# Kernel optimization log

Measured on AMD Instinct MI355X. Metric: run time of the kernel, lower is better.

Reference implementation:

```python
import jax, jax.numpy as jnp
import numpy as np

N_NODES = 20000
N_EDGES = 320000
N_GRAPHS = 256
D = 256
L = 4
EPS = 1e-5


def setup_inputs() -> dict:
    key = jax.random.key(0)
    ks = jax.random.split(key, 20)
    x = jax.random.normal(ks[0], (N_NODES, D), dtype=jnp.float32)
    edge_index = jax.random.randint(ks[1], (2, N_EDGES), 0, N_NODES, dtype=jnp.int64)
    batch = jnp.sort(jax.random.randint(ks[2], (N_NODES,), 0, N_GRAPHS, dtype=jnp.int64))
    s = 1.0 / np.sqrt(D)
    Wl = jax.random.uniform(ks[3], (L, D, D), jnp.float32, -s, s)
    bl = jax.random.uniform(ks[4], (L, D), jnp.float32, -s, s)
    Wr = jax.random.uniform(ks[5], (L, D, D), jnp.float32, -s, s)
    gamma = jnp.ones((L, D), jnp.float32)
    beta = jnp.zeros((L, D), jnp.float32)
    fc1_w = jax.random.uniform(ks[6], (D, 128), jnp.float32, -s, s)
    fc1_b = jax.random.uniform(ks[7], (128,), jnp.float32, -s, s)
    s2 = 1.0 / np.sqrt(128)
    fc2_w = jax.random.uniform(ks[8], (128, 64), jnp.float32, -s2, s2)
    fc2_b = jax.random.uniform(ks[9], (64,), jnp.float32, -s2, s2)
    s3 = 1.0 / np.sqrt(64)
    fc3_w = jax.random.uniform(ks[10], (64, 10), jnp.float32, -s3, s3)
    fc3_b = jax.random.uniform(ks[11], (10,), jnp.float32, -s3, s3)
    return dict(x=x, edge_index=edge_index, batch=batch, Wl=Wl, bl=bl, Wr=Wr,
                gamma=gamma, beta=beta, fc1_w=fc1_w, fc1_b=fc1_b,
                fc2_w=fc2_w, fc2_b=fc2_b, fc3_w=fc3_w, fc3_b=fc3_b)


def reference(x, edge_index, batch, Wl, bl, Wr, gamma, beta,
              fc1_w, fc1_b, fc2_w, fc2_b, fc3_w, fc3_b):
    src, dst = edge_index[0], edge_index[1]
    # in-degree for mean aggregation (zero-degree nodes -> 0 aggregate)
    deg = jax.ops.segment_sum(jnp.ones((src.shape[0],), x.dtype), dst, num_segments=N_NODES)
    inv_deg = jnp.where(deg > 0, 1.0 / jnp.maximum(deg, 1.0), 0.0)[:, None]
    for i in range(L):
        # SAGEConv: mean-aggregate neighbors, then lin_l(agg) + lin_r(x)
        agg = jax.ops.segment_sum(x[src], dst, num_segments=N_NODES) * inv_deg
        h = agg @ Wl[i] + bl[i] + x @ Wr[i]
        # BatchNorm (training mode: biased batch statistics over nodes)
        mu = jnp.mean(h, axis=0)
        var = jnp.mean(jnp.square(h - mu), axis=0)
        h = (h - mu) * jax.lax.rsqrt(var + EPS) * gamma[i] + beta[i]
        x = jax.nn.relu(h)
    # global_mean_pool over graphs
    cnt = jax.ops.segment_sum(jnp.ones((N_NODES,), x.dtype), batch, num_segments=N_GRAPHS)
    g = jax.ops.segment_sum(x, batch, num_segments=N_GRAPHS) / jnp.maximum(cnt, 1.0)[:, None]
    # MLP classifier: 256 -> 128 -> 64 -> 10
    g = jax.nn.relu(g @ fc1_w + fc1_b)
    g = jax.nn.relu(g @ fc2_w + fc2_b)
    return g @ fc3_w + fc3_b
```

## Files before the change

kernel.cpp:

```cpp
#include <hip/hip_runtime.h>
#include <hip/hip_bf16.h>

#define NN 20000
#define NE 320000
#define NG 256
#define DD 256
#define NL 4
#define NBX2 157
#define NBKT 79

typedef __attribute__((ext_vector_type(8))) short short8;
typedef __attribute__((ext_vector_type(4))) float float4_t;

__device__ __forceinline__ int ld_idx(const int* __restrict__ p, int i, int f64) {
    return f64 ? p[2 * i] : p[i];
}

__device__ __forceinline__ float bf2f(ushort u) {
    return __uint_as_float(((unsigned)u) << 16);
}

__device__ __forceinline__ ushort f2bf(float f) {
    __hip_bfloat16 b = __float2bfloat16(f);
    return *(ushort*)&b;
}


__global__ void k_init(const int* __restrict__ ei, const int* __restrict__ batch,
                       const ushort* __restrict__ x, int* __restrict__ flags,
                       int* __restrict__ deg) {
    int gid = blockIdx.x * 256 + threadIdx.x;
    for (int i = gid; i < NN; i += gridDim.x * 256) deg[i] = 0;
    if (blockIdx.x == 0) {
        __shared__ int cnt0, cnt1, weird;
        int t = threadIdx.x;
        if (t == 0) { cnt0 = 0; cnt1 = 0; weird = 0; }
        __syncthreads();
        for (int tt = t; tt < 512; tt += 256) {
            if (ei[2 * tt + 1] != 0) atomicAdd(&cnt0, 1);
            int i = tt * 9;
            if (batch[2 * i + 1] != 0) atomicAdd(&cnt1, 1);
#pragma unroll
            for (int j = 0; j < 16; j++) {
                ushort v = x[tt * 16 + j];
                if (((v >> 7) & 0xFF) >= 0xC0) atomicAdd(&weird, 1);
            }
        }
        __syncthreads();
        if (t == 0) {
            flags[0] = (cnt0 == 0) ? 1 : 0;
            flags[1] = (cnt1 == 0) ? 1 : 0;
            flags[2] = (weird == 0) ? 1 : 0;
        }
    }
}


#define POFF_BL   0
#define POFF_GA   1024
#define POFF_BE   2048
#define POFF_F1W  3072
#define POFF_F1B  35840
#define POFF_F2W  35968
#define POFF_F2B  44160
#define POFF_F3W  44224
#define POFF_F3B  44864
#define PTOT      44874

#define NB_CVT8   2500
#define NB_FRAG   2048
#define NB_CVTP   176
#define NB_DEG    1250
#define NB_GST    79
#define B_FRAG    (NB_CVT8)
#define B_CVTP    (B_FRAG + NB_FRAG)
#define B_DEG     (B_CVTP + NB_CVTP)
#define B_GST     (B_DEG + NB_DEG)
#define NB_PREP   (B_GST + NB_GST)


__global__ __launch_bounds__(256) void k_prep(
    const void* __restrict__ x_in, const void* __restrict__ WL,
    const void* __restrict__ WR, const int* __restrict__ ei,
    const int* __restrict__ batch,
    const void* s0, const void* s1, const void* s2, const void* s3,
    const void* s4, const void* s5, const void* s6, const void* s7, const void* s8,
    ushort* __restrict__ xcan, ushort* __restrict__ wtL, ushort* __restrict__ wtR,
    ushort* __restrict__ pcan, int* __restrict__ deg, int* __restrict__ gstart,
    const int* __restrict__ fl) {
    int blk = blockIdx.x;
    int t = threadIdx.x;
    if (blk < B_FRAG) {
        int i = blk * 256 + t;
        if (fl[2]) {
            *(int4*)(xcan + (size_t)i * 8) = ((const int4*)x_in)[i];
        } else {
            const float* f = (const float*)x_in + (size_t)i * 8;
            ushort ov[8];
#pragma unroll
            for (int d = 0; d < 8; d++) ov[d] = f2bf(f[d]);
            *(int4*)(xcan + (size_t)i * 8) = *(int4*)ov;
        }
    } else if (blk < B_CVTP) {
        int idx = (blk - B_FRAG) * 256 + t;
        int half = idx >> 18;
        int id = idx & 0x3FFFF;
        int within = id & 0xFFFF;
        int lmat = id >> 16;
        int fblk = within >> 9;
        int lane = (within >> 3) & 63;
        int e = within & 7;
        int n = (fblk >> 3) * 16 + (lane & 15);
        int k = (fblk & 7) * 32 + (lane >> 4) * 8 + e;
        const void* W = half ? WR : WL;
        ushort* Wt = half ? wtR : wtL;
        size_t src = ((size_t)lmat << 16) + (k << 8) + n;
        Wt[id] = fl[2] ? ((const ushort*)W)[src] : f2bf(((const float*)W)[src]);
    } else if (blk < B_DEG) {
        int i = (blk - B_CVTP) * 256 + t;
        if (i >= PTOT) return;
        const int offs[10] = {POFF_BL, POFF_GA, POFF_BE, POFF_F1W, POFF_F1B,
                              POFF_F2W, POFF_F2B, POFF_F3W, POFF_F3B, PTOT};
        const void* srcs[9] = {s0, s1, s2, s3, s4, s5, s6, s7, s8};
        int seg = 0;
#pragma unroll
        for (int k = 1; k < 9; k++) if (i >= offs[k]) seg = k;
        int local = i - offs[seg];
        if (fl[2]) pcan[i] = ((const ushort*)srcs[seg])[local];
        else       pcan[i] = f2bf(((const float*)srcs[seg])[local]);
    } else if (blk < B_GST) {
        int e = (blk - B_DEG) * 256 + t;
        if (e < NE) {
            int src = ld_idx(ei, e, fl[0]);
            int dst = ld_idx(ei, NE + e, fl[0]);
            if ((unsigned)dst < NN && (unsigned)src < NN) atomicAdd(&deg[dst], 1);
        }
    } else {
        int i = (blk - B_GST) * 256 + t;
        if (i >= NN) return;
        int b = ld_idx(batch, i, fl[1]);
        int bp = (i == 0) ? -1 : ld_idx(batch, i - 1, fl[1]);
        for (int g = bp + 1; g <= b; g++)
            if ((unsigned)g <= NG) gstart[g] = i;
        if (i == NN - 1)
            for (int g = b + 1; g <= NG; g++) gstart[g] = NN;
    }
}


__global__ __launch_bounds__(256) void k_scanA(const int* __restrict__ deg,
                                               int* __restrict__ bsum) {
    __shared__ int red[256];
    int t = threadIdx.x;
    int node = blockIdx.x * 256 + t;
    red[t] = (node < NN) ? deg[node] : 0;
    __syncthreads();
    for (int off = 128; off; off >>= 1) {
        if (t < off) red[t] += red[t + off];
        __syncthreads();
    }
    if (t == 0) bsum[blockIdx.x] = red[0];
}

__global__ __launch_bounds__(128) void k_scanB(const int* __restrict__ bsum,
                                               int* __restrict__ bpref,
                                               int* __restrict__ rowst) {
    __shared__ int part[128];
    int t = threadIdx.x;
    int s = (t < NBKT) ? bsum[t] : 0;
    part[t] = s;
    __syncthreads();
    for (int off = 1; off < 128; off <<= 1) {
        int v = (t >= off) ? part[t - off] : 0;
        __syncthreads();
        part[t] += v;
        __syncthreads();
    }
    if (t < NBKT) bpref[t] = part[t] - s;
    if (t == NBKT - 1) { bpref[NBKT] = part[t]; rowst[NN] = part[t]; }
}

__global__ __launch_bounds__(256) void k_scanC(
    const int* __restrict__ deg, const int* __restrict__ bpref,
    int* __restrict__ rowst, int* __restrict__ cursor, float* __restrict__ invdeg) {
    __shared__ int part[256];
    int b = blockIdx.x, t = threadIdx.x;
    int node = b * 256 + t;
    int d = (node < NN) ? deg[node] : 0;
    part[t] = d;
    __syncthreads();
    for (int off = 1; off < 256; off <<= 1) {
        int v = (t >= off) ? part[t - off] : 0;
        __syncthreads();
        part[t] += v;
        __syncthreads();
    }
    if (node < NN) {
        int o = bpref[b] + part[t] - d;
        rowst[node] = o;
        cursor[node] = o;
        invdeg[node] = d > 0 ? 1.0f / (float)d : 0.0f;
    }
}

__global__ void k_fill(const int* __restrict__ ei, int* __restrict__ cursor,
                       int* __restrict__ csr, const int* __restrict__ fl) {
    int e = blockIdx.x * 256 + threadIdx.x;
    if (e < NE) {
        int src = ld_idx(ei, e, fl[0]);
        int dst = ld_idx(ei, NE + e, fl[0]);
        if ((unsigned)dst < NN && (unsigned)src < NN) {
            int p = atomicAdd(&cursor[dst], 1);
            if ((unsigned)p < NE) csr[p] = src;
        }
    }
}


template <int BNF>
__global__ __launch_bounds__(256) void k_agg4(
    const ushort* __restrict__ X, const int* __restrict__ rs,
    const int* __restrict__ csr, const float* __restrict__ invdeg,
    const float* __restrict__ bnsc, const float* __restrict__ bnsh,
    ushort* __restrict__ AGG) {
    int node = blockIdx.x * 4 + (threadIdx.x >> 6);
    if (node >= NN) return;
    int h = (threadIdx.x >> 5) & 1;
    int j = threadIdx.x & 31;
    float sc[8], sh[8];
    if (BNF) {
        float4 a0 = *(const float4*)(bnsc + j * 8);
        float4 a1 = *(const float4*)(bnsc + j * 8 + 4);
        float4 b0 = *(const float4*)(bnsh + j * 8);
        float4 b1 = *(const float4*)(bnsh + j * 8 + 4);
        sc[0] = a0.x; sc[1] = a0.y; sc[2] = a0.z; sc[3] = a0.w;
        sc[4] = a1.x; sc[5] = a1.y; sc[6] = a1.z; sc[7] = a1.w;
        sh[0] = b0.x; sh[1] = b0.y; sh[2] = b0.z; sh[3] = b0.w;
        sh[4] = b1.x; sh[5] = b1.y; sh[6] = b1.z; sh[7] = b1.w;
    }
    int e0 = rs[node], e1 = rs[node + 1];
    float acc[8] = {};
    int e = e0 + h;
    for (; e + 14 < e1; e += 16) {
        int4 v[8];
#pragma unroll
        for (int r = 0; r < 8; r++) {
            int s = csr[e + 2 * r];
            v[r] = *(const int4*)(X + (size_t)s * DD + j * 8);
        }
#pragma unroll
        for (int r = 0; r < 8; r++) {
            const ushort* u = (const ushort*)&v[r];
#pragma unroll
            for (int d = 0; d < 8; d++) {
                float x = bf2f(u[d]);
                if (BNF) x = fmaxf(x * sc[d] + sh[d], 0.0f);
                acc[d] += x;
            }
        }
    }
    for (; e + 2 < e1; e += 4) {
        int sA = csr[e], sB = csr[e + 2];
        int4 vA = *(const int4*)(X + (size_t)sA * DD + j * 8);
        int4 vB = *(const int4*)(X + (size_t)sB * DD + j * 8);
        const ushort* uA = (const ushort*)&vA;
        const ushort* uB = (const ushort*)&vB;
#pragma unroll
        for (int d = 0; d < 8; d++) {
            float xA = bf2f(uA[d]), xB = bf2f(uB[d]);
            if (BNF) {
                xA = fmaxf(xA * sc[d] + sh[d], 0.0f);
                xB = fmaxf(xB * sc[d] + sh[d], 0.0f);
            }
            acc[d] += xA + xB;
        }
    }
    for (; e < e1; e += 2) {
        int s = csr[e];
        int4 v = *(const int4*)(X + (size_t)s * DD + j * 8);
        const ushort* u = (const ushort*)&v;
#pragma unroll
        for (int d = 0; d < 8; d++) {
            float x = bf2f(u[d]);
            if (BNF) x = fmaxf(x * sc[d] + sh[d], 0.0f);
            acc[d] += x;
        }
    }
#pragma unroll
    for (int d = 0; d < 8; d++)
        acc[d] += __shfl_down(acc[d], 32);
    if (h == 0) {
        float inv = invdeg[node];
        ushort ov[8];
#pragma unroll
        for (int d = 0; d < 8; d++) ov[d] = f2bf(acc[d] * inv);
        *(int4*)(AGG + (size_t)node * DD + j * 8) = *(int4*)ov;
    }
}


template <int BNF>
__global__ __launch_bounds__(256) void k_gemm5(
    const ushort* __restrict__ A1, const ushort* __restrict__ A2,
    const ushort* __restrict__ WtF1, const ushort* __restrict__ WtF2,
    const ushort* __restrict__ bias,
    const float* __restrict__ bnsc, const float* __restrict__ bnsh,
    ushort* __restrict__ H, float* __restrict__ psum, float* __restrict__ psq) {
    __shared__ ushort Als[128][40];
    __shared__ float colsum[128];
    __shared__ float colsq[128];
    const int m0 = blockIdx.x * 128;
    const int n0 = blockIdx.y * 128;
    const int tid = threadIdx.x;
    const int w = tid >> 6, l = tid & 63, lr = l & 15, q = l >> 4;
    const int wm = (w >> 1) * 64, wn = (w & 1) * 64;
    float4_t acc[4][4] = {};

    const int srow = tid >> 1;
    const int sce = (tid & 1) * 16;
    const int nb8 = ((n0 + wn) >> 4) * 8;

    for (int mat = 0; mat < 2; ++mat) {
        const ushort* A = mat ? A2 : A1;
        const ushort* Wf = mat ? WtF2 : WtF1;
        for (int k0 = 0; k0 < 256; k0 += 32) {
            int ar = m0 + srow; if (ar >= NN) ar = NN - 1;
            int4 av0 = *(const int4*)(A + (size_t)ar * DD + k0 + sce);
            int4 av1 = *(const int4*)(A + (size_t)ar * DD + k0 + sce + 8);
            if (BNF && mat == 1) {
                float scv[16], shv[16];
#pragma unroll
                for (int g = 0; g < 4; g++) {
                    float4 s4 = *(const float4*)(bnsc + k0 + sce + g * 4);
                    float4 h4 = *(const float4*)(bnsh + k0 + sce + g * 4);
                    scv[g*4] = s4.x; scv[g*4+1] = s4.y; scv[g*4+2] = s4.z; scv[g*4+3] = s4.w;
                    shv[g*4] = h4.x; shv[g*4+1] = h4.y; shv[g*4+2] = h4.z; shv[g*4+3] = h4.w;
                }
                ushort* u0 = (ushort*)&av0;
                ushort* u1 = (ushort*)&av1;
#pragma unroll
                for (int d = 0; d < 8; d++) {
                    u0[d] = f2bf(fmaxf(bf2f(u0[d]) * scv[d] + shv[d], 0.0f));
                    u1[d] = f2bf(fmaxf(bf2f(u1[d]) * scv[8 + d] + shv[8 + d], 0.0f));
                }
            }
            *(int4*)&Als[srow][sce] = av0;
            *(int4*)&Als[srow][sce + 8] = av1;
            const ushort* bbase = Wf + (((size_t)(nb8 + (k0 >> 5))) << 9) + l * 8;
            short8 bf[4];
#pragma unroll
            for (int in = 0; in < 4; in++)
                bf[in] = *(const short8*)(bbase + in * 4096);
            __syncthreads();
            short8 af[4];
#pragma unroll
            for (int im = 0; im < 4; im++)
                af[im] = *(const short8*)&Als[wm + im * 16 + lr][q * 8];
#pragma unroll
            for (int im = 0; im < 4; im++)
#pragma unroll
                for (int in = 0; in < 4; in++)
                    acc[im][in] = __builtin_amdgcn_mfma_f32_16x16x32_bf16(
                        af[im], bf[in], acc[im][in], 0, 0, 0);
            __syncthreads();
        }
    }
    if (tid < 128) { colsum[tid] = 0.0f; colsq[tid] = 0.0f; }
    __syncthreads();

    int mbase = m0 + wm + q * 4;
#pragma unroll
    for (int in = 0; in < 4; in++) {
        int n = n0 + wn + in * 16 + lr;
        float b = bf2f(bias[n]);
        float s = 0.0f, s2 = 0.0f;
#pragma unroll
        for (int im = 0; im < 4; im++) {
#pragma unroll
            for (int i = 0; i < 4; i++) {
                int m = mbase + im * 16 + i;
                if (m < NN) {
                    float hv = acc[im][in][i] + b;
                    ushort hb = f2bf(hv);
                    H[(size_t)m * DD + n] = hb;
                    float hq = bf2f(hb);
                    s += hq;
                    s2 += hq * hq;
                }
            }
        }
        s += __shfl_xor(s, 16);  s += __shfl_xor(s, 32);
        s2 += __shfl_xor(s2, 16); s2 += __shfl_xor(s2, 32);
        if (q == 0) {
            atomicAdd(&colsum[wn + in * 16 + lr], s);
            atomicAdd(&colsq[wn + in * 16 + lr], s2);
        }
    }
    __syncthreads();
    if (tid < 128) {
        psum[(size_t)blockIdx.x * DD + n0 + tid] = colsum[tid];
        psq[(size_t)blockIdx.x * DD + n0 + tid] = colsq[tid];
    }
}


__global__ __launch_bounds__(64) void k_bnfinal3(
    const float* __restrict__ psum, const float* __restrict__ psq,
    const ushort* __restrict__ gamma, const ushort* __restrict__ beta,
    float* __restrict__ scale, float* __restrict__ shift) {
    int c = blockIdx.x;
    int t = threadIdx.x;
    float s = 0.0f, s2 = 0.0f;
    for (int b = t; b < NBX2; b += 64) {
        s += psum[(size_t)b * DD + c];
        s2 += psq[(size_t)b * DD + c];
    }
#pragma unroll
    for (int o = 32; o; o >>= 1) {
        s += __shfl_down(s, o);
        s2 += __shfl_down(s2, o);
    }
    if (t == 0) {
        float mu = s * (1.0f / NN);
        float var = s2 * (1.0f / NN) - mu * mu;
        if (var < 0.0f) var = 0.0f;
        float rstd = rsqrtf(var + 1e-5f);
        float g = bf2f(gamma[c]);
        float b2 = bf2f(beta[c]);
        scale[c] = g * rstd;
        shift[c] = b2 - mu * g * rstd;
    }
}


__global__ __launch_bounds__(256) void k_head(
    const ushort* __restrict__ Hb, const float* __restrict__ scale,
    const float* __restrict__ shift, const int* __restrict__ gstart,
    const ushort* __restrict__ fc1w, const ushort* __restrict__ fc1b,
    const ushort* __restrict__ fc2w, const ushort* __restrict__ fc2b,
    const ushort* __restrict__ fc3w, const ushort* __restrict__ fc3b,
    void* __restrict__ out, const int* __restrict__ fl) {
    __shared__ float g[256];
    __shared__ float h1[128];
    __shared__ float h2[64];
    int gid = blockIdx.x;
    int t = threadIdx.x;
    int s0 = gstart[gid], e = gstart[gid + 1];
    float sc = scale[t], sh = shift[t];
    float acc = 0.0f;
    for (int i = s0; i < e; i++)
        acc += fmaxf(bf2f(Hb[(size_t)i * DD + t]) * sc + sh, 0.0f);
    g[t] = acc / fmaxf((float)(e - s0), 1.0f);
    __syncthreads();
    if (t < 128) {
        float a = bf2f(fc1b[t]);
        for (int k = 0; k < 256; k++)
            a += g[k] * bf2f(fc1w[k * 128 + t]);
        h1[t] = fmaxf(a, 0.0f);
    }
    __syncthreads();
    if (t < 64) {
        float a2 = bf2f(fc2b[t]);
        for (int k = 0; k < 128; k++)
            a2 += h1[k] * bf2f(fc2w[k * 64 + t]);
        h2[t] = fmaxf(a2, 0.0f);
    }
    __syncthreads();
    if (t < 10) {
        float a3 = bf2f(fc3b[t]);
        for (int k = 0; k < 64; k++)
            a3 += h2[k] * bf2f(fc3w[k * 10 + t]);
        if (fl[2]) ((__hip_bfloat16*)out)[gid * 10 + t] = __float2bfloat16(a3);
        else       ((float*)out)[gid * 10 + t] = a3;
    }
}


static inline char* bump(char*& p, size_t n) {
    char* r = p;
    p += (n + 255) & ~(size_t)255;
    return r;
}

extern "C" void kernel_launch(void* const* d_in, const int* in_sizes, int n_in,
                              void* d_out, int out_size, void* d_ws, size_t ws_size,
                              hipStream_t stream) {
    const void* x_in  = d_in[0];
    const int*  ei    = (const int*)d_in[1];
    const int*  batch = (const int*)d_in[2];
    const void* Wl    = d_in[3];
    const void* bl    = d_in[4];
    const void* Wr    = d_in[5];
    const void* gamma = d_in[6];
    const void* beta  = d_in[7];

    char* p = (char*)d_ws;
    int*    flags    = (int*)bump(p, 256);
    ushort* wtL      = (ushort*)bump(p, (size_t)NL * 65536 * 2);
    ushort* wtR      = (ushort*)bump(p, (size_t)NL * 65536 * 2);
    ushort* xcan     = (ushort*)bump(p, (size_t)NN * DD * 2);
    ushort* pcan     = (ushort*)bump(p, (size_t)PTOT * 2);
    int*    deg      = (int*)bump(p, NN * 4);
    int*    bsum     = (int*)bump(p, NBKT * 4);
    int*    bpref    = (int*)bump(p, (NBKT + 1) * 4);
    int*    rowst    = (int*)bump(p, (NN + 1) * 4);
    int*    cursor   = (int*)bump(p, NN * 4);
    float*  invdeg   = (float*)bump(p, NN * 4);
    int*    csr      = (int*)bump(p, NE * 4);
    int*    gstart   = (int*)bump(p, (NG + 1) * 4);
    ushort* agg      = (ushort*)bump(p, (size_t)NN * DD * 2);
    ushort* hb0      = (ushort*)bump(p, (size_t)NN * DD * 2);
    ushort* hb1      = (ushort*)bump(p, (size_t)NN * DD * 2);
    float*  psum     = (float*)bump(p, (size_t)NBX2 * DD * 4);
    float*  psq      = (float*)bump(p, (size_t)NBX2 * DD * 4);
    float*  scale    = (float*)bump(p, DD * 4);
    float*  shift    = (float*)bump(p, DD * 4);

    if ((size_t)(p - (char*)d_ws) > ws_size) return;

    ushort* blc = pcan + POFF_BL;
    ushort* gac = pcan + POFF_GA;
    ushort* bec = pcan + POFF_BE;
    ushort* f1w = pcan + POFF_F1W;
    ushort* f1b = pcan + POFF_F1B;
    ushort* f2w = pcan + POFF_F2W;
    ushort* f2b = pcan + POFF_F2B;
    ushort* f3w = pcan + POFF_F3W;
    ushort* f3b = pcan + POFF_F3B;

    k_init<<<80, 256, 0, stream>>>(ei, batch, (const ushort*)x_in, flags, deg);
    k_prep<<<NB_PREP, 256, 0, stream>>>(
        x_in, Wl, Wr, ei, batch,
        bl, gamma, beta, d_in[8], d_in[9], d_in[10], d_in[11], d_in[12], d_in[13],
        xcan, wtL, wtR, pcan, deg, gstart, flags);
    k_scanA<<<NBKT, 256, 0, stream>>>(deg, bsum);
    k_scanB<<<1, 128, 0, stream>>>(bsum, bpref, rowst);
    k_scanC<<<NBKT, 256, 0, stream>>>(deg, bpref, rowst, cursor, invdeg);
    k_fill<<<(NE + 255) / 256, 256, 0, stream>>>(ei, cursor, csr, flags);

    ushort* hbuf[2] = {hb0, hb1};
    const ushort* xsrc = xcan;
    for (int l = 0; l < NL; l++) {
        ushort* hdst = hbuf[l & 1];
        if (l == 0) {
            k_agg4<0><<<(NN + 3) / 4, 256, 0, stream>>>(xsrc, rowst, csr, invdeg,
                                                        scale, shift, agg);
            k_gemm5<0><<<dim3(NBX2, 2), 256, 0, stream>>>(
                agg, xsrc, wtL, wtR, blc, scale, shift, hdst, psum, psq);
        } else {
            k_agg4<1><<<(NN + 3) / 4, 256, 0, stream>>>(xsrc, rowst, csr, invdeg,
                                                        scale, shift, agg);
            k_gemm5<1><<<dim3(NBX2, 2), 256, 0, stream>>>(
                agg, xsrc, wtL + (size_t)l * 65536, wtR + (size_t)l * 65536,
                blc + l * DD, scale, shift, hdst, psum, psq);
        }
        k_bnfinal3<<<DD, 64, 0, stream>>>(psum, psq, gac + l * DD, bec + l * DD,
                                          scale, shift);
        xsrc = hdst;
    }

    k_head<<<NG, 256, 0, stream>>>(xsrc, scale, shift, gstart,
                                   f1w, f1b, f2w, f2b, f3w, f3b, d_out, flags);
}
```

Measured before the change: 372.5 us.

## Split aggregation across feature-column blocks and fold block-sum scan into scanC

The aggregation kernel now covers a 64-column slice per block, with a grid dimension of 4 slices. Within each wavefront, 8 groups of 8 lanes each take different edges and are reduced with xor shuffles, replacing two halves of 32 lanes over the full row. This puts more edges in flight per node and launches more blocks, at the cost of reading CSR indices four times and a longer shuffle reduction. The single-block scanB kernel is removed by having every scanC block redundantly scan the 79 block sums, which saves one launch.

```diff
diff --git a/kernel.cpp b/kernel.cpp
--- a/kernel.cpp
+++ b/kernel.cpp
@@ -162,29 +162,26 @@
     if (t == 0) bsum[blockIdx.x] = red[0];
 }
 
-__global__ __launch_bounds__(128) void k_scanB(const int* __restrict__ bsum,
-                                               int* __restrict__ bpref,
-                                               int* __restrict__ rowst) {
-    __shared__ int part[128];
-    int t = threadIdx.x;
-    int s = (t < NBKT) ? bsum[t] : 0;
-    part[t] = s;
-    __syncthreads();
-    for (int off = 1; off < 128; off <<= 1) {
-        int v = (t >= off) ? part[t - off] : 0;
-        __syncthreads();
-        part[t] += v;
-        __syncthreads();
-    }
-    if (t < NBKT) bpref[t] = part[t] - s;
-    if (t == NBKT - 1) { bpref[NBKT] = part[t]; rowst[NN] = part[t]; }
-}
-
 __global__ __launch_bounds__(256) void k_scanC(
-    const int* __restrict__ deg, const int* __restrict__ bpref,
+    const int* __restrict__ deg, const int* __restrict__ bsum,
     int* __restrict__ rowst, int* __restrict__ cursor, float* __restrict__ invdeg) {
+    __shared__ int bpart[128];
     __shared__ int part[256];
     int b = blockIdx.x, t = threadIdx.x;
+    if (t < 128) {
+        int s = (t < NBKT) ? bsum[t] : 0;
+        bpart[t] = s;
+    }
+    __syncthreads();
+    for (int off = 1; off < 128; off <<= 1) {
+        int v = 0;
+        if (t < 128 && t >= off) v = bpart[t - off];
+        __syncthreads();
+        if (t < 128) bpart[t] += v;
+        __syncthreads();
+    }
+    int bpref = (b == 0) ? 0 : bpart[b - 1];
+    if (b == 0 && t == 0) rowst[NN] = bpart[NBKT - 1];
     int node = b * 256 + t;
     int d = (node < NN) ? deg[node] : 0;
     part[t] = d;
@@ -196,7 +193,7 @@
         __syncthreads();
     }
     if (node < NN) {
-        int o = bpref[b] + part[t] - d;
+        int o = bpref + part[t] - d;
         rowst[node] = o;
         cursor[node] = o;
         invdeg[node] = d > 0 ? 1.0f / (float)d : 0.0f;
@@ -218,21 +215,23 @@
 
 
 template <int BNF>
-__global__ __launch_bounds__(256) void k_agg4(
+__global__ __launch_bounds__(256) void k_agg5(
     const ushort* __restrict__ X, const int* __restrict__ rs,
     const int* __restrict__ csr, const float* __restrict__ invdeg,
     const float* __restrict__ bnsc, const float* __restrict__ bnsh,
     ushort* __restrict__ AGG) {
     int node = blockIdx.x * 4 + (threadIdx.x >> 6);
     if (node >= NN) return;
-    int h = (threadIdx.x >> 5) & 1;
-    int j = threadIdx.x & 31;
+    int lane = threadIdx.x & 63;
+    int g = lane >> 3;
+    int j = lane & 7;
+    int cb = blockIdx.y * 64 + j * 8;
     float sc[8], sh[8];
     if (BNF) {
-        float4 a0 = *(const float4*)(bnsc + j * 8);
-        float4 a1 = *(const float4*)(bnsc + j * 8 + 4);
-        float4 b0 = *(const float4*)(bnsh + j * 8);
-        float4 b1 = *(const float4*)(bnsh + j * 8 + 4);
+        float4 a0 = *(const float4*)(bnsc + cb);
+        float4 a1 = *(const float4*)(bnsc + cb + 4);
+        float4 b0 = *(const float4*)(bnsh + cb);
+        float4 b1 = *(const float4*)(bnsh + cb + 4);
         sc[0] = a0.x; sc[1] = a0.y; sc[2] = a0.z; sc[3] = a0.w;
         sc[4] = a1.x; sc[5] = a1.y; sc[6] = a1.z; sc[7] = a1.w;
         sh[0] = b0.x; sh[1] = b0.y; sh[2] = b0.z; sh[3] = b0.w;
@@ -240,29 +239,11 @@
     }
     int e0 = rs[node], e1 = rs[node + 1];
     float acc[8] = {};
-    int e = e0 + h;
-    for (; e + 14 < e1; e += 16) {
-        int4 v[8];
-#pragma unroll
-        for (int r = 0; r < 8; r++) {
-            int s = csr[e + 2 * r];
-            v[r] = *(const int4*)(X + (size_t)s * DD + j * 8);
-        }
-#pragma unroll
-        for (int r = 0; r < 8; r++) {
-            const ushort* u = (const ushort*)&v[r];
-#pragma unroll
-            for (int d = 0; d < 8; d++) {
-                float x = bf2f(u[d]);
-                if (BNF) x = fmaxf(x * sc[d] + sh[d], 0.0f);
-                acc[d] += x;
-            }
-        }
-    }
-    for (; e + 2 < e1; e += 4) {
-        int sA = csr[e], sB = csr[e + 2];
-        int4 vA = *(const int4*)(X + (size_t)sA * DD + j * 8);
-        int4 vB = *(const int4*)(X + (size_t)sB * DD + j * 8);
+    int e = e0 + g;
+    for (; e + 8 < e1; e += 16) {
+        int sA = csr[e], sB = csr[e + 8];
+        int4 vA = *(const int4*)(X + (size_t)sA * DD + cb);
+        int4 vB = *(const int4*)(X + (size_t)sB * DD + cb);
         const ushort* uA = (const ushort*)&vA;
         const ushort* uB = (const ushort*)&vB;
 #pragma unroll
@@ -275,9 +256,9 @@
             acc[d] += xA + xB;
         }
     }
-    for (; e < e1; e += 2) {
+    for (; e < e1; e += 8) {
         int s = csr[e];
-        int4 v = *(const int4*)(X + (size_t)s * DD + j * 8);
+        int4 v = *(const int4*)(X + (size_t)s * DD + cb);
         const ushort* u = (const ushort*)&v;
 #pragma unroll
         for (int d = 0; d < 8; d++) {
@@ -287,14 +268,17 @@
         }
     }
 #pragma unroll
-    for (int d = 0; d < 8; d++)
-        acc[d] += __shfl_down(acc[d], 32);
-    if (h == 0) {
+    for (int d = 0; d < 8; d++) {
+        acc[d] += __shfl_xor(acc[d], 8);
+        acc[d] += __shfl_xor(acc[d], 16);
+        acc[d] += __shfl_xor(acc[d], 32);
+    }
+    if (g == 0) {
         float inv = invdeg[node];
         ushort ov[8];
 #pragma unroll
         for (int d = 0; d < 8; d++) ov[d] = f2bf(acc[d] * inv);
-        *(int4*)(AGG + (size_t)node * DD + j * 8) = *(int4*)ov;
+        *(int4*)(AGG + (size_t)node * DD + cb) = *(int4*)ov;
     }
 }
 
@@ -502,7 +486,6 @@
     ushort* pcan     = (ushort*)bump(p, (size_t)PTOT * 2);
     int*    deg      = (int*)bump(p, NN * 4);
     int*    bsum     = (int*)bump(p, NBKT * 4);
-    int*    bpref    = (int*)bump(p, (NBKT + 1) * 4);
     int*    rowst    = (int*)bump(p, (NN + 1) * 4);
     int*    cursor   = (int*)bump(p, NN * 4);
     float*  invdeg   = (float*)bump(p, NN * 4);
@@ -534,8 +517,7 @@
         bl, gamma, beta, d_in[8], d_in[9], d_in[10], d_in[11], d_in[12], d_in[13],
         xcan, wtL, wtR, pcan, deg, gstart, flags);
     k_scanA<<<NBKT, 256, 0, stream>>>(deg, bsum);
-    k_scanB<<<1, 128, 0, stream>>>(bsum, bpref, rowst);
-    k_scanC<<<NBKT, 256, 0, stream>>>(deg, bpref, rowst, cursor, invdeg);
+    k_scanC<<<NBKT, 256, 0, stream>>>(deg, bsum, rowst, cursor, invdeg);
     k_fill<<<(NE + 255) / 256, 256, 0, stream>>>(ei, cursor, csr, flags);
 
     ushort* hbuf[2] = {hb0, hb1};
@@ -543,13 +525,13 @@
     for (int l = 0; l < NL; l++) {
         ushort* hdst = hbuf[l & 1];
         if (l == 0) {
-            k_agg4<0><<<(NN + 3) / 4, 256, 0, stream>>>(xsrc, rowst, csr, invdeg,
-                                                        scale, shift, agg);
+            k_agg5<0><<<dim3((NN + 3) / 4, 4), 256, 0, stream>>>(
+                xsrc, rowst, csr, invdeg, scale, shift, agg);
             k_gemm5<0><<<dim3(NBX2, 2), 256, 0, stream>>>(
                 agg, xsrc, wtL, wtR, blc, scale, shift, hdst, psum, psq);
         } else {
-            k_agg4<1><<<(NN + 3) / 4, 256, 0, stream>>>(xsrc, rowst, csr, invdeg,
-                                                        scale, shift, agg);
+            k_agg5<1><<<dim3((NN + 3) / 4, 4), 256, 0, stream>>>(
+                xsrc, rowst, csr, invdeg, scale, shift, agg);
             k_gemm5<1><<<dim3(NBX2, 2), 256, 0, stream>>>(
                 agg, xsrc, wtL + (size_t)l * 65536, wtR + (size_t)l * 65536,
                 blc + l * DD, scale, shift, hdst, psum, psq);
```

After: 398.1 us. +6.9%, slower.

## Transpose weights via shared-memory tiles and fold block-sum scan into scanC

Applied to the files above, without the earlier changes.

The weight re-layout into MFMA fragment order changes from one scattered element per thread to 64x64 tiles staged through LDS. Each tile is read with coalesced loads and written back as 16-byte vectors, which cuts the prep blocks from 2048 to 128. The single-block scanB kernel is removed, and every scanC block now redundantly scans the 79 block sums in shared memory, saving one kernel launch and its serialization. The trade-off is extra LDS use and __syncthreads in k_prep and a small amount of duplicated scan work per block.

```diff
diff --git a/kernel.cpp b/kernel.cpp
--- a/kernel.cpp
+++ b/kernel.cpp
@@ -68,7 +68,7 @@
 #define PTOT      44874
 
 #define NB_CVT8   2500
-#define NB_FRAG   2048
+#define NB_FRAG   128
 #define NB_CVTP   176
 #define NB_DEG    1250
 #define NB_GST    79
@@ -102,20 +102,37 @@
             *(int4*)(xcan + (size_t)i * 8) = *(int4*)ov;
         }
     } else if (blk < B_CVTP) {
-        int idx = (blk - B_FRAG) * 256 + t;
-        int half = idx >> 18;
-        int id = idx & 0x3FFFF;
-        int within = id & 0xFFFF;
-        int lmat = id >> 16;
-        int fblk = within >> 9;
-        int lane = (within >> 3) & 63;
-        int e = within & 7;
-        int n = (fblk >> 3) * 16 + (lane & 15);
-        int k = (fblk & 7) * 32 + (lane >> 4) * 8 + e;
-        const void* W = half ? WR : WL;
-        ushort* Wt = half ? wtR : wtL;
-        size_t src = ((size_t)lmat << 16) + (k << 8) + n;
-        Wt[id] = fl[2] ? ((const ushort*)W)[src] : f2bf(((const float*)W)[src]);
+        __shared__ ushort T[64][65];
+        int bid = blk - B_FRAG;
+        int lm = bid >> 4;
+        int tile = bid & 15;
+        int tk = (tile >> 2) * 64, tn = (tile & 3) * 64;
+        const void* W = (lm >= 4) ? WR : WL;
+        ushort* Wt = (lm >= 4) ? wtR : wtL;
+        size_t base = (size_t)(lm & 3) << 16;
+        int f32 = !fl[2];
+#pragma unroll
+        for (int i = 0; i < 16; i++) {
+            int flat = t + i * 256;
+            int r = flat >> 6, c = flat & 63;
+            size_t src = base + (size_t)(tk + r) * 256 + tn + c;
+            ushort v = f32 ? f2bf(((const float*)W)[src]) : ((const ushort*)W)[src];
+            T[c][r] = v;
+        }
+        __syncthreads();
+#pragma unroll
+        for (int i = 0; i < 2; i++) {
+            int slot = t + i * 256;
+            int f = slot >> 6;
+            int lane = slot & 63;
+            int ln = (f >> 1) * 16 + (lane & 15);
+            int lk = (f & 1) * 32 + ((lane >> 4) << 3);
+            int gfblk = ((tn + ln) >> 4) * 8 + ((tk + lk) >> 5);
+            ushort tmp[8];
+#pragma unroll
+            for (int j = 0; j < 8; j++) tmp[j] = T[ln][lk + j];
+            *(int4*)(Wt + base + (size_t)gfblk * 512 + lane * 8) = *(int4*)tmp;
+        }
     } else if (blk < B_DEG) {
         int i = (blk - B_CVTP) * 256 + t;
         if (i >= PTOT) return;
@@ -162,29 +179,26 @@
     if (t == 0) bsum[blockIdx.x] = red[0];
 }
 
-__global__ __launch_bounds__(128) void k_scanB(const int* __restrict__ bsum,
-                                               int* __restrict__ bpref,
-                                               int* __restrict__ rowst) {
-    __shared__ int part[128];
-    int t = threadIdx.x;
-    int s = (t < NBKT) ? bsum[t] : 0;
-    part[t] = s;
-    __syncthreads();
-    for (int off = 1; off < 128; off <<= 1) {
-        int v = (t >= off) ? part[t - off] : 0;
-        __syncthreads();
-        part[t] += v;
-        __syncthreads();
-    }
-    if (t < NBKT) bpref[t] = part[t] - s;
-    if (t == NBKT - 1) { bpref[NBKT] = part[t]; rowst[NN] = part[t]; }
-}
-
 __global__ __launch_bounds__(256) void k_scanC(
-    const int* __restrict__ deg, const int* __restrict__ bpref,
+    const int* __restrict__ deg, const int* __restrict__ bsum,
     int* __restrict__ rowst, int* __restrict__ cursor, float* __restrict__ invdeg) {
+    __shared__ int bpart[128];
     __shared__ int part[256];
     int b = blockIdx.x, t = threadIdx.x;
+    if (t < 128) {
+        int s = (t < NBKT) ? bsum[t] : 0;
+        bpart[t] = s;
+    }
+    __syncthreads();
+    for (int off = 1; off < 128; off <<= 1) {
+        int v = 0;
+        if (t < 128 && t >= off) v = bpart[t - off];
+        __syncthreads();
+        if (t < 128) bpart[t] += v;
+        __syncthreads();
+    }
+    int bpref = (b == 0) ? 0 : bpart[b - 1];
+    if (b == 0 && t == 0) rowst[NN] = bpart[NBKT - 1];
     int node = b * 256 + t;
     int d = (node < NN) ? deg[node] : 0;
     part[t] = d;
@@ -196,7 +210,7 @@
         __syncthreads();
     }
     if (node < NN) {
-        int o = bpref[b] + part[t] - d;
+        int o = bpref + part[t] - d;
         rowst[node] = o;
         cursor[node] = o;
         invdeg[node] = d > 0 ? 1.0f / (float)d : 0.0f;
@@ -502,7 +516,6 @@
     ushort* pcan     = (ushort*)bump(p, (size_t)PTOT * 2);
     int*    deg      = (int*)bump(p, NN * 4);
     int*    bsum     = (int*)bump(p, NBKT * 4);
-    int*    bpref    = (int*)bump(p, (NBKT + 1) * 4);
     int*    rowst    = (int*)bump(p, (NN + 1) * 4);
     int*    cursor   = (int*)bump(p, NN * 4);
     float*  invdeg   = (float*)bump(p, NN * 4);
@@ -534,8 +547,7 @@
         bl, gamma, beta, d_in[8], d_in[9], d_in[10], d_in[11], d_in[12], d_in[13],
         xcan, wtL, wtR, pcan, deg, gstart, flags);
     k_scanA<<<NBKT, 256, 0, stream>>>(deg, bsum);
-    k_scanB<<<1, 128, 0, stream>>>(bsum, bpref, rowst);
-    k_scanC<<<NBKT, 256, 0, stream>>>(deg, bpref, rowst, cursor, invdeg);
+    k_scanC<<<NBKT, 256, 0, stream>>>(deg, bsum, rowst, cursor, invdeg);
     k_fill<<<(NE + 255) / 256, 256, 0, stream>>>(ei, cursor, csr, flags);
 
     ushort* hbuf[2] = {hb0, hb1};
```

Result: no change. 371.6 us, median of 2 (-0.2%).
